# Kernel tuning notes

Hardware: AMD Instinct MI355X
Metric: run time of the kernel (lower is better)

## Reference

```python
import jax, jax.numpy as jnp
import numpy as np
from jax import lax

T, H, K, V, O = 8192, 2048, 512, 512, 2048


def setup_inputs() -> dict:
    key = jax.random.key(0)
    ks = jax.random.split(key, 11)
    s_h = 1.0 / np.sqrt(H)
    s_v = 1.0 / np.sqrt(V)
    return {
        "hidden_state": jax.random.normal(ks[0], (T, H), jnp.float32),
        "Wq": jax.random.normal(ks[1], (H, K), jnp.float32) * s_h,
        "bq": jax.random.normal(ks[2], (K,), jnp.float32) * 0.02,
        "Wk": jax.random.normal(ks[3], (H, K), jnp.float32) * s_h,
        "bk": jax.random.normal(ks[4], (K,), jnp.float32) * 0.02,
        "Wv": jax.random.normal(ks[5], (H, V), jnp.float32) * s_h,
        "bv": jax.random.normal(ks[6], (V,), jnp.float32) * 0.02,
        "Wg": jax.random.normal(ks[7], (H, K), jnp.float32) * s_h,
        "bg": jax.random.normal(ks[8], (K,), jnp.float32) * 0.02,
        "Wo": jax.random.normal(ks[9], (V, O), jnp.float32) * s_v,
        "bo": jax.random.normal(ks[10], (O,), jnp.float32) * 0.02,
    }


def reference(hidden_state, Wq, bq, Wk, bk, Wv, bv, Wg, bg, Wo, bo):
    # Batched projections (torch Linear: x @ W^T + b; here W stored as [in,out])
    q = hidden_state @ Wq + bq                    # [T, K]
    k = jax.nn.sigmoid(hidden_state @ Wk + bk)    # [T, K]
    g = jax.nn.sigmoid(hidden_state @ Wg + bg)    # [T, K]
    v = hidden_state @ Wv + bv                    # [T, V]

    def step(state, qkvg):
        qi, ki, vi, gi = qkvg
        # state: [K, V]; gated decay per key-dim row, then outer-product write
        state = state * gi[:, None] + ki[:, None] * vi[None, :]
        out_i = qi @ state  # == state.T @ qi -> [V]
        return state, out_i

    init = jnp.zeros((K, V), hidden_state.dtype)
    final_state, outs = lax.scan(step, init, (q, k, v, g))  # outs: [T, V]
    output = outs @ Wo + bo                                  # [T, O]
    return output, final_state
```

## Files before the change

### kernel.cpp

```cpp
#include <hip/hip_runtime.h>

#define T_LEN 8192
#define H_DIM 2048
#define K_DIM 512
#define V_DIM 512
#define O_DIM 2048
#define CHUNK 64
#define NCHUNK 128
#define CGROUP 64

typedef short bf16x8 __attribute__((ext_vector_type(8)));
typedef float f32x4 __attribute__((ext_vector_type(4)));

typedef const __attribute__((address_space(1))) void* gptr1_t;
typedef __attribute__((address_space(3))) void* lptr3_t;

__device__ __forceinline__ float b2f(unsigned short u) {
    unsigned int i = ((unsigned int)u) << 16;
    float f;
    __builtin_memcpy(&f, &i, 4);
    return f;
}
__device__ __forceinline__ unsigned short f2b(float f) {
    unsigned int i;
    __builtin_memcpy(&i, &f, 4);
    unsigned int r = (i + 0x7FFFu + ((i >> 16) & 1u)) >> 16;
    return (unsigned short)r;
}
__device__ __forceinline__ float fw(float v) {
    return fminf(fmaxf(v, -1e30f), 1e30f);
}

__global__ __launch_bounds__(256) void conv2bf_k(const float* __restrict__ in,
                                                 unsigned short* __restrict__ out,
                                                 long N) {
    long i = ((long)blockIdx.x * 256 + threadIdx.x) * 8;
    if (i >= N) return;
    unsigned int w[4];
#pragma unroll
    for (int u = 0; u < 4; u++) {
        unsigned short lo = f2b(in[i + 2 * u]);
        unsigned short hi = f2b(in[i + 2 * u + 1]);
        w[u] = (unsigned int)lo | ((unsigned int)hi << 16);
    }
    uint4 pk; pk.x = w[0]; pk.y = w[1]; pk.z = w[2]; pk.w = w[3];
    *(uint4*)(out + i) = pk;
}

__global__ __launch_bounds__(64) void probe_k(int* __restrict__ flag) {
    __shared__ unsigned short As[16 * 32];
    __shared__ unsigned short Bs[16 * 32];
    int tid = threadIdx.x;
    for (int idx = tid; idx < 512; idx += 64) {
        int r = idx >> 5, c = idx & 31;
        float av = (c == 0) ? (float)(r + 1) : (c == 1 ? 1.0f : 0.0f);
        float bv = (c == 0) ? 1.0f : (c == 1 ? (float)(1024 * (r + 1)) : 0.0f);
        As[r * 32 + c] = f2b(av);
        Bs[r * 32 + c] = f2b(bv);
    }
    __syncthreads();
    int ln15 = tid & 15, q4 = (tid & 63) >> 4;
    bf16x8 a = *(const bf16x8*)(As + ln15 * 32 + q4 * 8);
    bf16x8 b = *(const bf16x8*)(Bs + ln15 * 32 + q4 * 8);
    f32x4 acc = {0.f, 0.f, 0.f, 0.f};
    acc = __builtin_amdgcn_mfma_f32_16x16x32_bf16(a, b, acc, 0, 0, 0);
    bool h0 = true, h1 = true;
#pragma unroll
    for (int i = 0; i < 4; i++) {
        float e0 = (float)((q4 * 4 + i + 1) + 1024 * (ln15 + 1));
        float e1 = (float)((ln15 + 1) + 1024 * (q4 * 4 + i + 1));
        h0 = h0 && (acc[i] == e0);
        h1 = h1 && (acc[i] == e1);
    }
    unsigned long long b0 = __ballot(h0 ? 1 : 0);
    unsigned long long b1 = __ballot(h1 ? 1 : 0);
    if (tid == 0) *flag = (b0 == ~0ull) ? 0 : ((b1 == ~0ull) ? 1 : 0);
}

template <int DF>
__global__ __launch_bounds__(256) void transpose_k(const void* __restrict__ in,
                                                   unsigned short* __restrict__ out,
                                                   int R, int C) {
    __shared__ unsigned short tile[32][33];
    int br = blockIdx.x, bc = blockIdx.y;
    int tc = threadIdx.x & 31, tr = threadIdx.x >> 5;
#pragma unroll
    for (int i = 0; i < 4; i++) {
        int r = tr + 8 * i;
        long idx = (long)(br * 32 + r) * C + bc * 32 + tc;
        tile[r][tc] = DF ? f2b(((const float*)in)[idx]) : ((const unsigned short*)in)[idx];
    }
    __syncthreads();
#pragma unroll
    for (int i = 0; i < 4; i++) {
        int r = tr + 8 * i;
        out[(long)(bc * 32 + r) * R + br * 32 + tc] = tile[tc][r];
    }
}

__global__ __launch_bounds__(512, 2) void proj_gemm256_k(const unsigned short* __restrict__ A,
                                                         const unsigned short* __restrict__ WT,
                                                         const float* __restrict__ bq,
                                                         const float* __restrict__ bk,
                                                         const float* __restrict__ bg,
                                                         const float* __restrict__ bv,
                                                         unsigned short* __restrict__ qb,
                                                         unsigned short* __restrict__ kb,
                                                         float* __restrict__ gb,
                                                         unsigned short* __restrict__ vT,
                                                         const int* __restrict__ flagp) {
    __shared__ unsigned short As[2][256 * 64];
    __shared__ unsigned short Bs[2][256 * 64];
    int fl = *flagp;
    int tid = threadIdx.x;
    int lane = tid & 63;
    int ln15 = lane & 15, q4 = lane >> 4;
    int w = tid >> 6;
    int wm = w >> 2, wn = w & 3;
    long m0 = (long)blockIdx.x * 256, n0 = (long)blockIdx.y * 256;

    int idx0 = tid, idx1 = 512 + tid;
    int r0_ = idx0 >> 3, r1_ = idx1 >> 3;
    int c80 = (idx0 & 7) ^ (r0_ & 7);
    int c81 = (idx1 & 7) ^ (r1_ & 7);
    int trA0 = ((r0_ >> 6) & 1) * 128 + (r0_ & 63);
    int trA1 = ((r1_ >> 6) & 1) * 128 + (r1_ & 63);
    int tcB0 = ((r0_ >> 5) & 3) * 64 + (r0_ & 31);
    int tcB1 = ((r1_ >> 5) & 3) * 64 + (r1_ & 31);
    const unsigned short* gA0 = A + (m0 + trA0) * (long)H_DIM + c80 * 8;
    const unsigned short* gA1 = A + (m0 + trA1) * (long)H_DIM + c81 * 8;
    const unsigned short* gB0 = WT + (n0 + tcB0) * (long)H_DIM + c80 * 8;
    const unsigned short* gB1 = WT + (n0 + tcB1) * (long)H_DIM + c81 * 8;
    int ld0 = idx0 * 8, ld1 = idx1 * 8;

#define STAGE_A(buf, half, ks)                                                              \
    do {                                                                                    \
        __builtin_amdgcn_global_load_lds(                                                   \
            (gptr1_t)(const void*)(gA0 + (long)(half) * 64 * H_DIM + (ks)),                 \
            (lptr3_t)(void*)(&As[buf][(half) * 8192 + ld0]), 16, 0, 0);                     \
        __builtin_amdgcn_global_load_lds(                                                   \
            (gptr1_t)(const void*)(gA1 + (long)(half) * 64 * H_DIM + (ks)),                 \
            (lptr3_t)(void*)(&As[buf][(half) * 8192 + ld1]), 16, 0, 0);                     \
    } while (0)
#define STAGE_B(buf, half, ks)                                                              \
    do {                                                                                    \
        __builtin_amdgcn_global_load_lds(                                                   \
            (gptr1_t)(const void*)(gB0 + (long)(half) * 32 * H_DIM + (ks)),                 \
            (lptr3_t)(void*)(&Bs[buf][(half) * 8192 + ld0]), 16, 0, 0);                     \
        __builtin_amdgcn_global_load_lds(                                                   \
            (gptr1_t)(const void*)(gB1 + (long)(half) * 32 * H_DIM + (ks)),                 \
            (lptr3_t)(void*)(&Bs[buf][(half) * 8192 + ld1]), 16, 0, 0);                     \
    } while (0)

    auto LDA = [&](int buf, int im, int s) -> bf16x8 {
        int row = (im >> 2) * 128 + wm * 64 + (im & 3) * 16 + ln15;
        int cb = (s * 64 + q4 * 16) ^ ((row & 7) << 4);
        return *(const bf16x8*)((const unsigned short*)As[buf] + row * 64 + (cb >> 1));
    };
    auto LDB = [&](int buf, int jn, int s) -> bf16x8 {
        int row = (jn >> 1) * 128 + wn * 32 + (jn & 1) * 16 + ln15;
        int cb = (s * 64 + q4 * 16) ^ ((row & 7) << 4);
        return *(const bf16x8*)((const unsigned short*)Bs[buf] + row * 64 + (cb >> 1));
    };

    f32x4 acc[8][4] = {};

    STAGE_A(0, 0, 0);
    STAGE_B(0, 0, 0);
    STAGE_B(0, 1, 0);
    STAGE_A(0, 1, 0);
    STAGE_A(1, 0, 64);
    STAGE_B(1, 0, 64);
    asm volatile("s_waitcnt vmcnt(4)" ::: "memory");
    __builtin_amdgcn_s_barrier();

    int cur = 0;
    for (int kt = 0; kt < H_DIM; kt += 64, cur ^= 1) {
        int k1 = (kt + 64) & (H_DIM - 1);
        int k2 = (kt + 128) & (H_DIM - 1);
        bf16x8 af[4][2], blo[2][2], bhi[2][2];

#pragma unroll
        for (int i = 0; i < 4; i++) { af[i][0] = LDA(cur, i, 0); af[i][1] = LDA(cur, i, 1); }
#pragma unroll
        for (int j = 0; j < 2; j++) { blo[j][0] = LDB(cur, j, 0); blo[j][1] = LDB(cur, j, 1); }
        STAGE_B(cur ^ 1, 1, k1);
        __builtin_amdgcn_s_barrier();
        asm volatile("s_waitcnt lgkmcnt(0)" ::: "memory");
        __builtin_amdgcn_sched_barrier(0);
        __builtin_amdgcn_s_setprio(1);
#pragma unroll
        for (int i = 0; i < 4; i++)
#pragma unroll
            for (int j = 0; j < 2; j++) {
                acc[i][j] = __builtin_amdgcn_mfma_f32_16x16x32_bf16(af[i][0], blo[j][0], acc[i][j], 0, 0, 0);
                acc[i][j] = __builtin_amdgcn_mfma_f32_16x16x32_bf16(af[i][1], blo[j][1], acc[i][j], 0, 0, 0);
            }
        __builtin_amdgcn_s_setprio(0);
        __builtin_amdgcn_s_barrier();

#pragma unroll
        for (int j = 0; j < 2; j++) { bhi[j][0] = LDB(cur, 2 + j, 0); bhi[j][1] = LDB(cur, 2 + j, 1); }
        STAGE_A(cur ^ 1, 1, k1);
        __builtin_amdgcn_s_barrier();
        asm volatile("s_waitcnt lgkmcnt(0)" ::: "memory");
        __builtin_amdgcn_sched_barrier(0);
        __builtin_amdgcn_s_setprio(1);
#pragma unroll
        for (int i = 0; i < 4; i++)
#pragma unroll
            for (int j = 0; j < 2; j++) {
                acc[i][2 + j] = __builtin_amdgcn_mfma_f32_16x16x32_bf16(af[i][0], bhi[j][0], acc[i][2 + j], 0, 0, 0);
                acc[i][2 + j] = __builtin_amdgcn_mfma_f32_16x16x32_bf16(af[i][1], bhi[j][1], acc[i][2 + j], 0, 0, 0);
            }
        __builtin_amdgcn_s_setprio(0);
        __builtin_amdgcn_s_barrier();

#pragma unroll
        for (int i = 0; i < 4; i++) { af[i][0] = LDA(cur, 4 + i, 0); af[i][1] = LDA(cur, 4 + i, 1); }
        STAGE_A(cur, 0, k2);
        __builtin_amdgcn_s_barrier();
        asm volatile("s_waitcnt lgkmcnt(0)" ::: "memory");
        __builtin_amdgcn_sched_barrier(0);
        __builtin_amdgcn_s_setprio(1);
#pragma unroll
        for (int i = 0; i < 4; i++)
#pragma unroll
            for (int j = 0; j < 2; j++) {
                acc[4 + i][2 + j] = __builtin_amdgcn_mfma_f32_16x16x32_bf16(af[i][0], bhi[j][0], acc[4 + i][2 + j], 0, 0, 0);
                acc[4 + i][2 + j] = __builtin_amdgcn_mfma_f32_16x16x32_bf16(af[i][1], bhi[j][1], acc[4 + i][2 + j], 0, 0, 0);
            }
        __builtin_amdgcn_s_setprio(0);
        __builtin_amdgcn_s_barrier();

        STAGE_B(cur, 0, k2);
        __builtin_amdgcn_s_setprio(1);
#pragma unroll
        for (int i = 0; i < 4; i++)
#pragma unroll
            for (int j = 0; j < 2; j++) {
                acc[4 + i][j] = __builtin_amdgcn_mfma_f32_16x16x32_bf16(af[i][0], blo[j][0], acc[4 + i][j], 0, 0, 0);
                acc[4 + i][j] = __builtin_amdgcn_mfma_f32_16x16x32_bf16(af[i][1], blo[j][1], acc[4 + i][j], 0, 0, 0);
            }
        __builtin_amdgcn_s_setprio(0);
        asm volatile("s_waitcnt vmcnt(4)" ::: "memory");
        __builtin_amdgcn_s_barrier();
    }

    int seg = (int)(n0 >> 9);
    int nl0 = (int)(n0 & 511);
    const float* bias = seg == 0 ? bq : seg == 1 ? bk : seg == 2 ? bg : bv;

    if (seg == 3 && fl == 0) {
#pragma unroll
        for (int im = 0; im < 8; im++)
#pragma unroll
            for (int jn = 0; jn < 4; jn++) {
                int nl = nl0 + wn * 64 + (jn >> 1) * 32 + (jn & 1) * 16 + ln15;
                float bsv = bias[nl];
                long mb = m0 + wm * 128 + (im >> 2) * 64 + (im & 3) * 16 + q4 * 4;
                unsigned short h0 = f2b(fw(acc[im][jn][0] + bsv));
                unsigned short h1 = f2b(fw(acc[im][jn][1] + bsv));
                unsigned short h2 = f2b(fw(acc[im][jn][2] + bsv));
                unsigned short h3 = f2b(fw(acc[im][jn][3] + bsv));
                uint2 pk;
                pk.x = (unsigned int)h0 | ((unsigned int)h1 << 16);
                pk.y = (unsigned int)h2 | ((unsigned int)h3 << 16);
                *(uint2*)(vT + (long)nl * T_LEN + mb) = pk;
            }
    } else {
#pragma unroll
        for (int im = 0; im < 8; im++)
#pragma unroll
            for (int jn = 0; jn < 4; jn++)
#pragma unroll
                for (int ii = 0; ii < 4; ii++) {
                    int dm = fl ? ln15 : q4 * 4 + ii;
                    int dn = fl ? q4 * 4 + ii : ln15;
                    long m = m0 + wm * 128 + (im >> 2) * 64 + (im & 3) * 16 + dm;
                    int nl = nl0 + wn * 64 + (jn >> 1) * 32 + (jn & 1) * 16 + dn;
                    float v = fw(acc[im][jn][ii] + bias[nl]);
                    if (seg == 1 || seg == 2) v = 1.0f / (1.0f + __expf(-v));
                    if (seg == 0)
                        qb[m * K_DIM + nl] = f2b(v);
                    else if (seg == 1)
                        kb[m * K_DIM + nl] = f2b(v);
                    else if (seg == 2)
                        gb[m * K_DIM + nl] = v;
                    else
                        vT[(long)nl * T_LEN + m] = f2b(v);
                }
    }
#undef STAGE_A
#undef STAGE_B
}

__global__ __launch_bounds__(256) void gemm_f32_k(const unsigned short* __restrict__ A,
                                                  const unsigned short* __restrict__ BT,
                                                  const float* __restrict__ bias,
                                                  float* __restrict__ out,
                                                  int M, int N, int K,
                                                  const int* __restrict__ flagp) {
    __shared__ unsigned short As[128 * 32];
    __shared__ unsigned short Bs[128 * 32];
    int fl = *flagp;
    int tid = threadIdx.x;
    int lane = tid & 63;
    int w = tid >> 6;
    int ln15 = lane & 15, q4 = lane >> 4;
    int wm = w >> 1, wn = w & 1;
    long m0 = (long)blockIdx.x * 128, n0 = (long)blockIdx.y * 128;

    f32x4 acc[4][4] = {};

    for (int kt = 0; kt < K; kt += 32) {
        __syncthreads();
#pragma unroll
        for (int it = 0; it < 2; it++) {
            int chunk = it * 256 + tid;
            int row = chunk >> 2;
            int col = (chunk & 3) * 8;
            const unsigned short* ga = A + (m0 + row) * (long)K + kt + col;
            const unsigned short* gbp = BT + (n0 + row) * (long)K + kt + col;
            __builtin_amdgcn_global_load_lds((gptr1_t)(const void*)ga,
                                             (lptr3_t)(void*)(As + chunk * 8), 16, 0, 0);
            __builtin_amdgcn_global_load_lds((gptr1_t)(const void*)gbp,
                                             (lptr3_t)(void*)(Bs + chunk * 8), 16, 0, 0);
        }
        __syncthreads();
        bf16x8 a[4], b[4];
#pragma unroll
        for (int i = 0; i < 4; i++)
            a[i] = *(const bf16x8*)(As + (wm * 64 + 16 * i + ln15) * 32 + q4 * 8);
#pragma unroll
        for (int j = 0; j < 4; j++)
            b[j] = *(const bf16x8*)(Bs + (wn * 64 + 16 * j + ln15) * 32 + q4 * 8);
#pragma unroll
        for (int i = 0; i < 4; i++)
#pragma unroll
            for (int j = 0; j < 4; j++)
                acc[i][j] = __builtin_amdgcn_mfma_f32_16x16x32_bf16(a[i], b[j], acc[i][j], 0, 0, 0);
    }

#pragma unroll
    for (int i = 0; i < 4; i++)
#pragma unroll
        for (int j = 0; j < 4; j++)
#pragma unroll
            for (int ii = 0; ii < 4; ii++) {
                int dm = fl ? ln15 : q4 * 4 + ii;
                int dn = fl ? q4 * 4 + ii : ln15;
                long m = m0 + wm * 64 + 16 * i + dm;
                long n = n0 + wn * 64 + 16 * j + dn;
                out[m * N + n] = fw(acc[i][j][ii] + bias[n]);
            }
}

__global__ __launch_bounds__(256) void cumprod_k(const float* __restrict__ g,
                                                 unsigned short* __restrict__ q,
                                                 unsigned short* __restrict__ k,
                                                 unsigned short* __restrict__ khatT,
                                                 float* __restrict__ pend) {
    int c = blockIdx.x;
    int d = blockIdx.y * 256 + threadIdx.x;
    long base = (long)c * CHUNK * K_DIM + d;
    float P = 1.0f;
    for (int s = 0; s < CHUNK; s++) P = fmaxf(P * g[base + (long)s * K_DIM], 1e-37f);
    pend[c * K_DIM + d] = P;
    float Pend = P;
    P = 1.0f;
    for (int s8 = 0; s8 < CHUNK; s8 += 8) {
        unsigned int packed[4];
#pragma unroll
        for (int u = 0; u < 8; u++) {
            int s = s8 + u;
            long idx = base + (long)s * K_DIM;
            P = fmaxf(P * g[idx], 1e-37f);
            float qv = fw(b2f(q[idx]) * P);
            q[idx] = f2b(qv);
            float kv = b2f(k[idx]);
            float kt = kv / P;
            kt = fmaxf(fminf(kt, 3e37f), -3e37f);
            k[idx] = f2b(kt);
            float ratio = Pend / P;
            unsigned short kh = f2b(fw(kv * ratio));
            if (u & 1)
                packed[u >> 1] |= ((unsigned int)kh) << 16;
            else
                packed[u >> 1] = kh;
        }
        uint4 pk;
        pk.x = packed[0]; pk.y = packed[1]; pk.z = packed[2]; pk.w = packed[3];
        *(uint4*)(khatT + (long)d * T_LEN + c * CHUNK + s8) = pk;
    }
}

__global__ __launch_bounds__(256) void scan_k(const unsigned short* __restrict__ khatT,
                                              const unsigned short* __restrict__ vT,
                                              const float* __restrict__ pend,
                                              unsigned short* __restrict__ ST,
                                              float* __restrict__ Sio,
                                              int c0, int cn,
                                              const int* __restrict__ flagp) {
    int fl = *flagp;
    int lane = threadIdx.x & 63, w = threadIdx.x >> 6;
    int ln15 = lane & 15, q4 = lane >> 4;
    int k0 = (blockIdx.x & 15) * 32 + (w & 1) * 16;
    int v0 = (blockIdx.x >> 4) * 32 + (w >> 1) * 16;
    f32x4 acc;
#pragma unroll
    for (int i = 0; i < 4; i++) {
        int dk = fl ? ln15 : q4 * 4 + i;
        int dv = fl ? q4 * 4 + i : ln15;
        acc[i] = Sio[(long)(k0 + dk) * V_DIM + v0 + dv];
    }
    for (int c = c0; c < cn; c++) {
        long cloc = c - c0;
        if (!fl) {
            uint2 pk;
            pk.x = (unsigned int)f2b(fw(acc[0])) | ((unsigned int)f2b(fw(acc[1])) << 16);
            pk.y = (unsigned int)f2b(fw(acc[2])) | ((unsigned int)f2b(fw(acc[3])) << 16);
            *(uint2*)(ST + (cloc * V_DIM + v0 + ln15) * K_DIM + k0 + q4 * 4) = pk;
            float4 pd = *(const float4*)(pend + c * K_DIM + k0 + q4 * 4);
            acc[0] *= pd.x; acc[1] *= pd.y; acc[2] *= pd.z; acc[3] *= pd.w;
        } else {
#pragma unroll
            for (int i = 0; i < 4; i++)
                ST[(cloc * V_DIM + v0 + q4 * 4 + i) * K_DIM + k0 + ln15] = f2b(fw(acc[i]));
            float pd = pend[c * K_DIM + k0 + ln15];
#pragma unroll
            for (int i = 0; i < 4; i++) acc[i] *= pd;
        }
#pragma unroll
        for (int s0 = 0; s0 < CHUNK; s0 += 32) {
            bf16x8 a = *(const bf16x8*)(khatT + (long)(k0 + ln15) * T_LEN + c * CHUNK + s0 + q4 * 8);
            bf16x8 b = *(const bf16x8*)(vT + (long)(v0 + ln15) * T_LEN + c * CHUNK + s0 + q4 * 8);
            acc = __builtin_amdgcn_mfma_f32_16x16x32_bf16(a, b, acc, 0, 0, 0);
        }
    }
#pragma unroll
    for (int i = 0; i < 4; i++) {
        int dk = fl ? ln15 : q4 * 4 + i;
        int dv = fl ? q4 * 4 + i : ln15;
        Sio[(long)(k0 + dk) * V_DIM + v0 + dv] = fw(acc[i]);
    }
}

__global__ __launch_bounds__(256) void copy_state_k(const float* __restrict__ S,
                                                    float* __restrict__ out) {
    long i = (long)blockIdx.x * 1024 + threadIdx.x * 4;
    *(float4*)(out + i) = *(const float4*)(S + i);
}

__global__ __launch_bounds__(256) void intra_k(const unsigned short* __restrict__ qs,
                                               const unsigned short* __restrict__ ks,
                                               const unsigned short* __restrict__ vT,
                                               const unsigned short* __restrict__ ST,
                                               unsigned short* __restrict__ outs,
                                               int c_base,
                                               const int* __restrict__ flagp) {
    __shared__ unsigned short Ab[64 * 72];
    int fl = *flagp;
    long cloc = blockIdx.x >> 1;
    int c = c_base + (int)cloc, h = blockIdx.x & 1;
    int lane = threadIdx.x & 63, w = threadIdx.x >> 6;
    int ln15 = lane & 15, q4 = lane >> 4;
    long t0 = (long)c * CHUNK;

    {
        f32x4 accA[4] = {};
        for (int kk = 0; kk < K_DIM; kk += 32) {
            bf16x8 a = *(const bf16x8*)(qs + (t0 + 16 * w + ln15) * K_DIM + kk + q4 * 8);
#pragma unroll
            for (int j = 0; j < 4; j++) {
                bf16x8 b = *(const bf16x8*)(ks + (t0 + 16 * j + ln15) * K_DIM + kk + q4 * 8);
                accA[j] = __builtin_amdgcn_mfma_f32_16x16x32_bf16(a, b, accA[j], 0, 0, 0);
            }
        }
#pragma unroll
        for (int j = 0; j < 4; j++)
#pragma unroll
            for (int i = 0; i < 4; i++) {
                int dt = fl ? ln15 : q4 * 4 + i;
                int ds = fl ? q4 * 4 + i : ln15;
                int tl = 16 * w + dt;
                int s = 16 * j + ds;
                float av = (s <= tl) ? accA[j][i] : 0.0f;
                Ab[tl * 72 + s] = f2b(fw(av));
            }
    }
    __syncthreads();

    int v0 = h * 256 + w * 64;
    f32x4 acc[4][4] = {};
    for (int kk = 0; kk < K_DIM; kk += 32) {
        bf16x8 a[4], b[4];
#pragma unroll
        for (int i = 0; i < 4; i++)
            a[i] = *(const bf16x8*)(qs + (t0 + 16 * i + ln15) * K_DIM + kk + q4 * 8);
#pragma unroll
        for (int j = 0; j < 4; j++)
            b[j] = *(const bf16x8*)(ST + (cloc * V_DIM + v0 + 16 * j + ln15) * K_DIM + kk + q4 * 8);
#pragma unroll
        for (int i = 0; i < 4; i++)
#pragma unroll
            for (int j = 0; j < 4; j++)
                acc[i][j] = __builtin_amdgcn_mfma_f32_16x16x32_bf16(a[i], b[j], acc[i][j], 0, 0, 0);
    }
#pragma unroll
    for (int s0 = 0; s0 < CHUNK; s0 += 32) {
        bf16x8 a[4], b[4];
#pragma unroll
        for (int i = 0; i < 4; i++)
            a[i] = *(const bf16x8*)(Ab + (16 * i + ln15) * 72 + s0 + q4 * 8);
#pragma unroll
        for (int j = 0; j < 4; j++)
            b[j] = *(const bf16x8*)(vT + (long)(v0 + 16 * j + ln15) * T_LEN + t0 + s0 + q4 * 8);
#pragma unroll
        for (int i = 0; i < 4; i++)
#pragma unroll
            for (int j = 0; j < 4; j++)
                acc[i][j] = __builtin_amdgcn_mfma_f32_16x16x32_bf16(a[i], b[j], acc[i][j], 0, 0, 0);
    }
#pragma unroll
    for (int i = 0; i < 4; i++)
#pragma unroll
        for (int j = 0; j < 4; j++)
#pragma unroll
            for (int ii = 0; ii < 4; ii++) {
                int dt = fl ? ln15 : q4 * 4 + ii;
                int dv = fl ? q4 * 4 + ii : ln15;
                outs[(t0 + 16 * i + dt) * V_DIM + v0 + 16 * j + dv] = f2b(fw(acc[i][j][ii]));
            }
}

extern "C" void kernel_launch(void* const* d_in, const int* in_sizes, int n_in,
                              void* d_out, int out_size, void* d_ws, size_t ws_size,
                              hipStream_t stream) {
    const float* hs = (const float*)d_in[0];
    const float* Wq = (const float*)d_in[1];
    const float* bq = (const float*)d_in[2];
    const float* Wk = (const float*)d_in[3];
    const float* bk = (const float*)d_in[4];
    const float* Wv = (const float*)d_in[5];
    const float* bv = (const float*)d_in[6];
    const float* Wg = (const float*)d_in[7];
    const float* bg = (const float*)d_in[8];
    const float* Wo = (const float*)d_in[9];
    const float* bo = (const float*)d_in[10];

    float* out = (float*)d_out;

    char* ws = (char*)d_ws;
    const size_t MB = 1024 * 1024;
    unsigned short* WT = (unsigned short*)(ws + 0 * MB);
    unsigned short* WoT = (unsigned short*)(ws + 8 * MB);
    unsigned short* qb = (unsigned short*)(ws + 10 * MB);
    unsigned short* kb = (unsigned short*)(ws + 18 * MB);
    unsigned short* vTb = (unsigned short*)(ws + 26 * MB);
    float* gb = (float*)(ws + 34 * MB);
    unsigned short* outsb = (unsigned short*)(ws + 34 * MB);
    unsigned short* khatT = (unsigned short*)(ws + 50 * MB);
    float* pend = (float*)(ws + 58 * MB);
    int* flags = (int*)(ws + 58 * MB + 256 * 1024);
    float* Scarry = (float*)(ws + 59 * MB);
    unsigned short* STb = (unsigned short*)(ws + 60 * MB);
    unsigned short* hsb = (unsigned short*)(ws + 60 * MB);
    float* fsspare = (float*)(ws + 92 * MB);
    (void)ws_size; (void)in_sizes; (void)n_in;

    float* finalst =
        ((long)out_size >= (long)T_LEN * O_DIM + (long)K_DIM * V_DIM)
            ? out + (long)T_LEN * O_DIM
            : fsspare;

    dim3 b256(256);
    hipMemsetAsync(flags, 0, 16, stream);
    probe_k<<<dim3(1), dim3(64), 0, stream>>>(flags);
    conv2bf_k<<<dim3(8192), b256, 0, stream>>>(hs, hsb, (long)T_LEN * H_DIM);
    transpose_k<1><<<dim3(H_DIM / 32, K_DIM / 32), b256, 0, stream>>>(Wq, WT + 0 * 512 * H_DIM, H_DIM, K_DIM);
    transpose_k<1><<<dim3(H_DIM / 32, K_DIM / 32), b256, 0, stream>>>(Wk, WT + 1 * 512 * H_DIM, H_DIM, K_DIM);
    transpose_k<1><<<dim3(H_DIM / 32, K_DIM / 32), b256, 0, stream>>>(Wg, WT + 2 * 512 * H_DIM, H_DIM, K_DIM);
    transpose_k<1><<<dim3(H_DIM / 32, V_DIM / 32), b256, 0, stream>>>(Wv, WT + 3 * 512 * H_DIM, H_DIM, V_DIM);
    transpose_k<1><<<dim3(V_DIM / 32, O_DIM / 32), b256, 0, stream>>>(Wo, WoT, V_DIM, O_DIM);
    proj_gemm256_k<<<dim3(T_LEN / 256, 8), dim3(512), 0, stream>>>(
        hsb, WT, bq, bk, bg, bv, qb, kb, gb, vTb, flags);
    cumprod_k<<<dim3(NCHUNK, K_DIM / 256), b256, 0, stream>>>(gb, qb, kb, khatT, pend);
    hipMemsetAsync(Scarry, 0, (size_t)K_DIM * V_DIM * 4, stream);
    scan_k<<<dim3(256), b256, 0, stream>>>(khatT, vTb, pend, STb, Scarry, 0, CGROUP, flags);
    intra_k<<<dim3(2 * CGROUP), b256, 0, stream>>>(qb, kb, vTb, STb, outsb, 0, flags);
    scan_k<<<dim3(256), b256, 0, stream>>>(khatT, vTb, pend, STb, Scarry, CGROUP, NCHUNK, flags);
    intra_k<<<dim3(2 * CGROUP), b256, 0, stream>>>(qb, kb, vTb, STb, outsb, CGROUP, flags);
    copy_state_k<<<dim3((K_DIM * V_DIM) / 1024), b256, 0, stream>>>(Scarry, finalst);
    gemm_f32_k<<<dim3(T_LEN / 128, O_DIM / 128), b256, 0, stream>>>(
        outsb, WoT, bo, out, T_LEN, O_DIM, V_DIM, flags);
}
```

Baseline: 455.7 us.

## Fuse prep kernels, single-pass scan with prefetch, and 256-tile output GEMM

Merges the bf16 conversion and the five weight transposes into one prep kernel, which saves launches. The chunk scan now runs in a single pass with register prefetch of the next four chunks, removing the two-group split, the carry memset and the state copy kernel. The output projection moves to a 256x256 double-buffered LDS GEMM like the projection kernel, and cumprod caches the gate products in registers. The explicit lgkmcnt waits and sched barriers are replaced with a plain s_barrier macro, which could risk LDS read ordering.

```diff
diff --git a/kernel.cpp b/kernel.cpp
--- a/kernel.cpp
+++ b/kernel.cpp
@@ -7,7 +7,6 @@
 #define O_DIM 2048
 #define CHUNK 64
 #define NCHUNK 128
-#define CGROUP 64
 
 typedef short bf16x8 __attribute__((ext_vector_type(8)));
 typedef float f32x4 __attribute__((ext_vector_type(4)));
@@ -31,21 +30,7 @@
     return fminf(fmaxf(v, -1e30f), 1e30f);
 }
 
-__global__ __launch_bounds__(256) void conv2bf_k(const float* __restrict__ in,
-                                                 unsigned short* __restrict__ out,
-                                                 long N) {
-    long i = ((long)blockIdx.x * 256 + threadIdx.x) * 8;
-    if (i >= N) return;
-    unsigned int w[4];
-#pragma unroll
-    for (int u = 0; u < 4; u++) {
-        unsigned short lo = f2b(in[i + 2 * u]);
-        unsigned short hi = f2b(in[i + 2 * u + 1]);
-        w[u] = (unsigned int)lo | ((unsigned int)hi << 16);
-    }
-    uint4 pk; pk.x = w[0]; pk.y = w[1]; pk.z = w[2]; pk.w = w[3];
-    *(uint4*)(out + i) = pk;
-}
+#define BARX() asm volatile("s_barrier" ::: "memory")
 
 __global__ __launch_bounds__(64) void probe_k(int* __restrict__ flag) {
     __shared__ unsigned short As[16 * 32];
@@ -77,24 +62,53 @@
     if (tid == 0) *flag = (b0 == ~0ull) ? 0 : ((b1 == ~0ull) ? 1 : 0);
 }
 
-template <int DF>
-__global__ __launch_bounds__(256) void transpose_k(const void* __restrict__ in,
-                                                   unsigned short* __restrict__ out,
-                                                   int R, int C) {
+__global__ __launch_bounds__(256) void prep_k(const float* __restrict__ hs,
+                                              unsigned short* __restrict__ hsb,
+                                              const float* __restrict__ Wq,
+                                              const float* __restrict__ Wk,
+                                              const float* __restrict__ Wg,
+                                              const float* __restrict__ Wv,
+                                              const float* __restrict__ Wo,
+                                              unsigned short* __restrict__ WT,
+                                              unsigned short* __restrict__ WoT) {
     __shared__ unsigned short tile[32][33];
-    int br = blockIdx.x, bc = blockIdx.y;
-    int tc = threadIdx.x & 31, tr = threadIdx.x >> 5;
+    long bid = blockIdx.x;
+    int tid = threadIdx.x;
+    if (bid < 8192) {
+        long i = (bid * 256 + tid) * 8;
+        unsigned int wd[4];
+#pragma unroll
+        for (int u = 0; u < 4; u++) {
+            unsigned short lo = f2b(hs[i + 2 * u]);
+            unsigned short hi = f2b(hs[i + 2 * u + 1]);
+            wd[u] = (unsigned int)lo | ((unsigned int)hi << 16);
+        }
+        uint4 pk; pk.x = wd[0]; pk.y = wd[1]; pk.z = wd[2]; pk.w = wd[3];
+        *(uint4*)(hsb + i) = pk;
+        return;
+    }
+    int t = (int)(bid - 8192);
+    int mat = t >> 10, tl = t & 1023;
+    const float* in; unsigned short* outp; int R, C, br, bc;
+    if (mat < 4) {
+        in = mat == 0 ? Wq : mat == 1 ? Wk : mat == 2 ? Wg : Wv;
+        outp = WT + (long)mat * 512 * H_DIM;
+        R = H_DIM; C = 512; br = tl >> 4; bc = tl & 15;
+    } else {
+        in = Wo; outp = WoT; R = V_DIM; C = O_DIM; br = tl & 15; bc = tl >> 4;
+    }
+    int tc = tid & 31, tr = tid >> 5;
 #pragma unroll
     for (int i = 0; i < 4; i++) {
         int r = tr + 8 * i;
         long idx = (long)(br * 32 + r) * C + bc * 32 + tc;
-        tile[r][tc] = DF ? f2b(((const float*)in)[idx]) : ((const unsigned short*)in)[idx];
+        tile[r][tc] = f2b(in[idx]);
     }
     __syncthreads();
 #pragma unroll
     for (int i = 0; i < 4; i++) {
         int r = tr + 8 * i;
-        out[(long)(bc * 32 + r) * R + br * 32 + tc] = tile[tc][r];
+        outp[(long)(bc * 32 + r) * R + br * 32 + tc] = tile[tc][r];
     }
 }
 
@@ -172,7 +186,7 @@
     STAGE_A(1, 0, 64);
     STAGE_B(1, 0, 64);
     asm volatile("s_waitcnt vmcnt(4)" ::: "memory");
-    __builtin_amdgcn_s_barrier();
+    BARX();
 
     int cur = 0;
     for (int kt = 0; kt < H_DIM; kt += 64, cur ^= 1) {
@@ -185,9 +199,7 @@
 #pragma unroll
         for (int j = 0; j < 2; j++) { blo[j][0] = LDB(cur, j, 0); blo[j][1] = LDB(cur, j, 1); }
         STAGE_B(cur ^ 1, 1, k1);
-        __builtin_amdgcn_s_barrier();
-        asm volatile("s_waitcnt lgkmcnt(0)" ::: "memory");
-        __builtin_amdgcn_sched_barrier(0);
+        BARX();
         __builtin_amdgcn_s_setprio(1);
 #pragma unroll
         for (int i = 0; i < 4; i++)
@@ -197,14 +209,12 @@
                 acc[i][j] = __builtin_amdgcn_mfma_f32_16x16x32_bf16(af[i][1], blo[j][1], acc[i][j], 0, 0, 0);
             }
         __builtin_amdgcn_s_setprio(0);
-        __builtin_amdgcn_s_barrier();
+        BARX();
 
 #pragma unroll
         for (int j = 0; j < 2; j++) { bhi[j][0] = LDB(cur, 2 + j, 0); bhi[j][1] = LDB(cur, 2 + j, 1); }
         STAGE_A(cur ^ 1, 1, k1);
-        __builtin_amdgcn_s_barrier();
-        asm volatile("s_waitcnt lgkmcnt(0)" ::: "memory");
-        __builtin_amdgcn_sched_barrier(0);
+        BARX();
         __builtin_amdgcn_s_setprio(1);
 #pragma unroll
         for (int i = 0; i < 4; i++)
@@ -214,14 +224,12 @@
                 acc[i][2 + j] = __builtin_amdgcn_mfma_f32_16x16x32_bf16(af[i][1], bhi[j][1], acc[i][2 + j], 0, 0, 0);
             }
         __builtin_amdgcn_s_setprio(0);
-        __builtin_amdgcn_s_barrier();
+        BARX();
 
 #pragma unroll
         for (int i = 0; i < 4; i++) { af[i][0] = LDA(cur, 4 + i, 0); af[i][1] = LDA(cur, 4 + i, 1); }
         STAGE_A(cur, 0, k2);
-        __builtin_amdgcn_s_barrier();
-        asm volatile("s_waitcnt lgkmcnt(0)" ::: "memory");
-        __builtin_amdgcn_sched_barrier(0);
+        BARX();
         __builtin_amdgcn_s_setprio(1);
 #pragma unroll
         for (int i = 0; i < 4; i++)
@@ -231,7 +239,7 @@
                 acc[4 + i][2 + j] = __builtin_amdgcn_mfma_f32_16x16x32_bf16(af[i][1], bhi[j][1], acc[4 + i][2 + j], 0, 0, 0);
             }
         __builtin_amdgcn_s_setprio(0);
-        __builtin_amdgcn_s_barrier();
+        BARX();
 
         STAGE_B(cur, 0, k2);
         __builtin_amdgcn_s_setprio(1);
@@ -244,7 +252,7 @@
             }
         __builtin_amdgcn_s_setprio(0);
         asm volatile("s_waitcnt vmcnt(4)" ::: "memory");
-        __builtin_amdgcn_s_barrier();
+        BARX();
     }
 
     int seg = (int)(n0 >> 9);
@@ -295,65 +303,158 @@
 #undef STAGE_B
 }
 
-__global__ __launch_bounds__(256) void gemm_f32_k(const unsigned short* __restrict__ A,
-                                                  const unsigned short* __restrict__ BT,
-                                                  const float* __restrict__ bias,
-                                                  float* __restrict__ out,
-                                                  int M, int N, int K,
-                                                  const int* __restrict__ flagp) {
-    __shared__ unsigned short As[128 * 32];
-    __shared__ unsigned short Bs[128 * 32];
+__global__ __launch_bounds__(512, 2) void gemm256_k(const unsigned short* __restrict__ A,
+                                                    const unsigned short* __restrict__ BT,
+                                                    const float* __restrict__ bias,
+                                                    float* __restrict__ out,
+                                                    int N, int KT,
+                                                    const int* __restrict__ flagp) {
+    __shared__ unsigned short As[2][256 * 64];
+    __shared__ unsigned short Bs[2][256 * 64];
     int fl = *flagp;
     int tid = threadIdx.x;
     int lane = tid & 63;
+    int ln15 = lane & 15, q4 = lane >> 4;
     int w = tid >> 6;
-    int ln15 = lane & 15, q4 = lane >> 4;
-    int wm = w >> 1, wn = w & 1;
-    long m0 = (long)blockIdx.x * 128, n0 = (long)blockIdx.y * 128;
-
-    f32x4 acc[4][4] = {};
-
-    for (int kt = 0; kt < K; kt += 32) {
-        __syncthreads();
-#pragma unroll
-        for (int it = 0; it < 2; it++) {
-            int chunk = it * 256 + tid;
-            int row = chunk >> 2;
-            int col = (chunk & 3) * 8;
-            const unsigned short* ga = A + (m0 + row) * (long)K + kt + col;
-            const unsigned short* gbp = BT + (n0 + row) * (long)K + kt + col;
-            __builtin_amdgcn_global_load_lds((gptr1_t)(const void*)ga,
-                                             (lptr3_t)(void*)(As + chunk * 8), 16, 0, 0);
-            __builtin_amdgcn_global_load_lds((gptr1_t)(const void*)gbp,
-                                             (lptr3_t)(void*)(Bs + chunk * 8), 16, 0, 0);
-        }
-        __syncthreads();
-        bf16x8 a[4], b[4];
-#pragma unroll
-        for (int i = 0; i < 4; i++)
-            a[i] = *(const bf16x8*)(As + (wm * 64 + 16 * i + ln15) * 32 + q4 * 8);
-#pragma unroll
-        for (int j = 0; j < 4; j++)
-            b[j] = *(const bf16x8*)(Bs + (wn * 64 + 16 * j + ln15) * 32 + q4 * 8);
-#pragma unroll
-        for (int i = 0; i < 4; i++)
-#pragma unroll
-            for (int j = 0; j < 4; j++)
-                acc[i][j] = __builtin_amdgcn_mfma_f32_16x16x32_bf16(a[i], b[j], acc[i][j], 0, 0, 0);
-    }
-
-#pragma unroll
-    for (int i = 0; i < 4; i++)
-#pragma unroll
-        for (int j = 0; j < 4; j++)
+    int wm = w >> 2, wn = w & 3;
+    long m0 = (long)blockIdx.x * 256, n0 = (long)blockIdx.y * 256;
+
+    int idx0 = tid, idx1 = 512 + tid;
+    int r0_ = idx0 >> 3, r1_ = idx1 >> 3;
+    int c80 = (idx0 & 7) ^ (r0_ & 7);
+    int c81 = (idx1 & 7) ^ (r1_ & 7);
+    int trA0 = ((r0_ >> 6) & 1) * 128 + (r0_ & 63);
+    int trA1 = ((r1_ >> 6) & 1) * 128 + (r1_ & 63);
+    int tcB0 = ((r0_ >> 5) & 3) * 64 + (r0_ & 31);
+    int tcB1 = ((r1_ >> 5) & 3) * 64 + (r1_ & 31);
+    const unsigned short* gA0 = A + (m0 + trA0) * (long)KT + c80 * 8;
+    const unsigned short* gA1 = A + (m0 + trA1) * (long)KT + c81 * 8;
+    const unsigned short* gB0 = BT + (n0 + tcB0) * (long)KT + c80 * 8;
+    const unsigned short* gB1 = BT + (n0 + tcB1) * (long)KT + c81 * 8;
+    int ld0 = idx0 * 8, ld1 = idx1 * 8;
+
+#define STAGE_A(buf, half, ks)                                                              \
+    do {                                                                                    \
+        __builtin_amdgcn_global_load_lds(                                                   \
+            (gptr1_t)(const void*)(gA0 + (long)(half) * 64 * KT + (ks)),                    \
+            (lptr3_t)(void*)(&As[buf][(half) * 8192 + ld0]), 16, 0, 0);                     \
+        __builtin_amdgcn_global_load_lds(                                                   \
+            (gptr1_t)(const void*)(gA1 + (long)(half) * 64 * KT + (ks)),                    \
+            (lptr3_t)(void*)(&As[buf][(half) * 8192 + ld1]), 16, 0, 0);                     \
+    } while (0)
+#define STAGE_B(buf, half, ks)                                                              \
+    do {                                                                                    \
+        __builtin_amdgcn_global_load_lds(                                                   \
+            (gptr1_t)(const void*)(gB0 + (long)(half) * 32 * KT + (ks)),                    \
+            (lptr3_t)(void*)(&Bs[buf][(half) * 8192 + ld0]), 16, 0, 0);                     \
+        __builtin_amdgcn_global_load_lds(                                                   \
+            (gptr1_t)(const void*)(gB1 + (long)(half) * 32 * KT + (ks)),                    \
+            (lptr3_t)(void*)(&Bs[buf][(half) * 8192 + ld1]), 16, 0, 0);                     \
+    } while (0)
+
+    auto LDA = [&](int buf, int im, int s) -> bf16x8 {
+        int row = (im >> 2) * 128 + wm * 64 + (im & 3) * 16 + ln15;
+        int cb = (s * 64 + q4 * 16) ^ ((row & 7) << 4);
+        return *(const bf16x8*)((const unsigned short*)As[buf] + row * 64 + (cb >> 1));
+    };
+    auto LDB = [&](int buf, int jn, int s) -> bf16x8 {
+        int row = (jn >> 1) * 128 + wn * 32 + (jn & 1) * 16 + ln15;
+        int cb = (s * 64 + q4 * 16) ^ ((row & 7) << 4);
+        return *(const bf16x8*)((const unsigned short*)Bs[buf] + row * 64 + (cb >> 1));
+    };
+
+    f32x4 acc[8][4] = {};
+
+    STAGE_A(0, 0, 0);
+    STAGE_B(0, 0, 0);
+    STAGE_B(0, 1, 0);
+    STAGE_A(0, 1, 0);
+    STAGE_A(1, 0, 64);
+    STAGE_B(1, 0, 64);
+    asm volatile("s_waitcnt vmcnt(4)" ::: "memory");
+    BARX();
+
+    int cur = 0;
+    for (int kt = 0; kt < KT; kt += 64, cur ^= 1) {
+        int k1 = (kt + 64) & (KT - 1);
+        int k2 = (kt + 128) & (KT - 1);
+        bf16x8 af[4][2], blo[2][2], bhi[2][2];
+
+#pragma unroll
+        for (int i = 0; i < 4; i++) { af[i][0] = LDA(cur, i, 0); af[i][1] = LDA(cur, i, 1); }
+#pragma unroll
+        for (int j = 0; j < 2; j++) { blo[j][0] = LDB(cur, j, 0); blo[j][1] = LDB(cur, j, 1); }
+        STAGE_B(cur ^ 1, 1, k1);
+        BARX();
+        __builtin_amdgcn_s_setprio(1);
+#pragma unroll
+        for (int i = 0; i < 4; i++)
+#pragma unroll
+            for (int j = 0; j < 2; j++) {
+                acc[i][j] = __builtin_amdgcn_mfma_f32_16x16x32_bf16(af[i][0], blo[j][0], acc[i][j], 0, 0, 0);
+                acc[i][j] = __builtin_amdgcn_mfma_f32_16x16x32_bf16(af[i][1], blo[j][1], acc[i][j], 0, 0, 0);
+            }
+        __builtin_amdgcn_s_setprio(0);
+        BARX();
+
+#pragma unroll
+        for (int j = 0; j < 2; j++) { bhi[j][0] = LDB(cur, 2 + j, 0); bhi[j][1] = LDB(cur, 2 + j, 1); }
+        STAGE_A(cur ^ 1, 1, k1);
+        BARX();
+        __builtin_amdgcn_s_setprio(1);
+#pragma unroll
+        for (int i = 0; i < 4; i++)
+#pragma unroll
+            for (int j = 0; j < 2; j++) {
+                acc[i][2 + j] = __builtin_amdgcn_mfma_f32_16x16x32_bf16(af[i][0], bhi[j][0], acc[i][2 + j], 0, 0, 0);
+                acc[i][2 + j] = __builtin_amdgcn_mfma_f32_16x16x32_bf16(af[i][1], bhi[j][1], acc[i][2 + j], 0, 0, 0);
+            }
+        __builtin_amdgcn_s_setprio(0);
+        BARX();
+
+#pragma unroll
+        for (int i = 0; i < 4; i++) { af[i][0] = LDA(cur, 4 + i, 0); af[i][1] = LDA(cur, 4 + i, 1); }
+        STAGE_A(cur, 0, k2);
+        BARX();
+        __builtin_amdgcn_s_setprio(1);
+#pragma unroll
+        for (int i = 0; i < 4; i++)
+#pragma unroll
+            for (int j = 0; j < 2; j++) {
+                acc[4 + i][2 + j] = __builtin_amdgcn_mfma_f32_16x16x32_bf16(af[i][0], bhi[j][0], acc[4 + i][2 + j], 0, 0, 0);
+                acc[4 + i][2 + j] = __builtin_amdgcn_mfma_f32_16x16x32_bf16(af[i][1], bhi[j][1], acc[4 + i][2 + j], 0, 0, 0);
+            }
+        __builtin_amdgcn_s_setprio(0);
+        BARX();
+
+        STAGE_B(cur, 0, k2);
+        __builtin_amdgcn_s_setprio(1);
+#pragma unroll
+        for (int i = 0; i < 4; i++)
+#pragma unroll
+            for (int j = 0; j < 2; j++) {
+                acc[4 + i][j] = __builtin_amdgcn_mfma_f32_16x16x32_bf16(af[i][0], blo[j][0], acc[4 + i][j], 0, 0, 0);
+                acc[4 + i][j] = __builtin_amdgcn_mfma_f32_16x16x32_bf16(af[i][1], blo[j][1], acc[4 + i][j], 0, 0, 0);
+            }
+        __builtin_amdgcn_s_setprio(0);
+        asm volatile("s_waitcnt vmcnt(4)" ::: "memory");
+        BARX();
+    }
+
+#pragma unroll
+    for (int im = 0; im < 8; im++)
+#pragma unroll
+        for (int jn = 0; jn < 4; jn++)
 #pragma unroll
             for (int ii = 0; ii < 4; ii++) {
                 int dm = fl ? ln15 : q4 * 4 + ii;
                 int dn = fl ? q4 * 4 + ii : ln15;
-                long m = m0 + wm * 64 + 16 * i + dm;
-                long n = n0 + wn * 64 + 16 * j + dn;
-                out[m * N + n] = fw(acc[i][j][ii] + bias[n]);
-            }
+                long m = m0 + wm * 128 + (im >> 2) * 64 + (im & 3) * 16 + dm;
+                long n = n0 + wn * 64 + (jn >> 1) * 32 + (jn & 1) * 16 + dn;
+                out[m * N + n] = fw(acc[im][jn][ii] + bias[n]);
+            }
+#undef STAGE_A
+#undef STAGE_B
 }
 
 __global__ __launch_bounds__(256) void cumprod_k(const float* __restrict__ g,
@@ -364,25 +465,29 @@
     int c = blockIdx.x;
     int d = blockIdx.y * 256 + threadIdx.x;
     long base = (long)c * CHUNK * K_DIM + d;
+    float gv[CHUNK];
+#pragma unroll
+    for (int s = 0; s < CHUNK; s++) gv[s] = g[base + (long)s * K_DIM];
     float P = 1.0f;
-    for (int s = 0; s < CHUNK; s++) P = fmaxf(P * g[base + (long)s * K_DIM], 1e-37f);
+#pragma unroll
+    for (int s = 0; s < CHUNK; s++) { P = fmaxf(P * gv[s], 1e-37f); gv[s] = P; }
     pend[c * K_DIM + d] = P;
     float Pend = P;
-    P = 1.0f;
+#pragma unroll
     for (int s8 = 0; s8 < CHUNK; s8 += 8) {
         unsigned int packed[4];
 #pragma unroll
         for (int u = 0; u < 8; u++) {
             int s = s8 + u;
             long idx = base + (long)s * K_DIM;
-            P = fmaxf(P * g[idx], 1e-37f);
-            float qv = fw(b2f(q[idx]) * P);
+            float Pc = gv[s];
+            float qv = fw(b2f(q[idx]) * Pc);
             q[idx] = f2b(qv);
             float kv = b2f(k[idx]);
-            float kt = kv / P;
+            float kt = kv / Pc;
             kt = fmaxf(fminf(kt, 3e37f), -3e37f);
             k[idx] = f2b(kt);
-            float ratio = Pend / P;
+            float ratio = Pend / Pc;
             unsigned short kh = f2b(fw(kv * ratio));
             if (u & 1)
                 packed[u >> 1] |= ((unsigned int)kh) << 16;
@@ -399,57 +504,73 @@
                                               const unsigned short* __restrict__ vT,
                                               const float* __restrict__ pend,
                                               unsigned short* __restrict__ ST,
-                                              float* __restrict__ Sio,
-                                              int c0, int cn,
+                                              float* __restrict__ fstate,
                                               const int* __restrict__ flagp) {
     int fl = *flagp;
     int lane = threadIdx.x & 63, w = threadIdx.x >> 6;
     int ln15 = lane & 15, q4 = lane >> 4;
     int k0 = (blockIdx.x & 15) * 32 + (w & 1) * 16;
     int v0 = (blockIdx.x >> 4) * 32 + (w >> 1) * 16;
-    f32x4 acc;
+    f32x4 acc = {0.f, 0.f, 0.f, 0.f};
+    const unsigned short* kb_ = khatT + (long)(k0 + ln15) * T_LEN + q4 * 8;
+    const unsigned short* vb_ = vT + (long)(v0 + ln15) * T_LEN + q4 * 8;
+
+    bf16x8 kf0[2], vf0[2], kf1[2], vf1[2], kf2[2], vf2[2], kf3[2], vf3[2];
+    float4 pdv[4];
+    float pds[4];
+
+#define LOADSET(s, c)                                                        \
+    do {                                                                     \
+        long off_ = (long)(c) * CHUNK;                                       \
+        kf##s[0] = *(const bf16x8*)(kb_ + off_);                             \
+        kf##s[1] = *(const bf16x8*)(kb_ + off_ + 32);                        \
+        vf##s[0] = *(const bf16x8*)(vb_ + off_);                             \
+        vf##s[1] = *(const bf16x8*)(vb_ + off_ + 32);                        \
+        if (!fl)                                                             \
+            pdv[s] = *(const float4*)(pend + (c) * K_DIM + k0 + q4 * 4);     \
+        else                                                                 \
+            pds[s] = pend[(c) * K_DIM + k0 + ln15];                          \
+    } while (0)
+
+    LOADSET(0, 0); LOADSET(1, 1); LOADSET(2, 2); LOADSET(3, 3);
+
+#define STEP(s, c)                                                                             \
+    do {                                                                                       \
+        if (!fl) {                                                                             \
+            uint2 pk_;                                                                         \
+            pk_.x = (unsigned int)f2b(fw(acc[0])) | ((unsigned int)f2b(fw(acc[1])) << 16);     \
+            pk_.y = (unsigned int)f2b(fw(acc[2])) | ((unsigned int)f2b(fw(acc[3])) << 16);     \
+            *(uint2*)(ST + ((long)(c) * V_DIM + v0 + ln15) * K_DIM + k0 + q4 * 4) = pk_;       \
+            acc[0] *= pdv[s].x; acc[1] *= pdv[s].y; acc[2] *= pdv[s].z; acc[3] *= pdv[s].w;    \
+        } else {                                                                               \
+            ST[((long)(c) * V_DIM + v0 + q4 * 4 + 0) * K_DIM + k0 + ln15] = f2b(fw(acc[0]));   \
+            ST[((long)(c) * V_DIM + v0 + q4 * 4 + 1) * K_DIM + k0 + ln15] = f2b(fw(acc[1]));   \
+            ST[((long)(c) * V_DIM + v0 + q4 * 4 + 2) * K_DIM + k0 + ln15] = f2b(fw(acc[2]));   \
+            ST[((long)(c) * V_DIM + v0 + q4 * 4 + 3) * K_DIM + k0 + ln15] = f2b(fw(acc[3]));   \
+            acc[0] *= pds[s]; acc[1] *= pds[s]; acc[2] *= pds[s]; acc[3] *= pds[s];            \
+        }                                                                                      \
+        acc = __builtin_amdgcn_mfma_f32_16x16x32_bf16(kf##s[0], vf##s[0], acc, 0, 0, 0);       \
+        acc = __builtin_amdgcn_mfma_f32_16x16x32_bf16(kf##s[1], vf##s[1], acc, 0, 0, 0);       \
+        int cp_ = (c) + 4;                                                                     \
+        if (cp_ > NCHUNK - 1) cp_ = NCHUNK - 1;                                                \
+        LOADSET(s, cp_);                                                                       \
+    } while (0)
+
+    for (int c = 0; c < NCHUNK; c += 4) {
+        STEP(0, c);
+        STEP(1, c + 1);
+        STEP(2, c + 2);
+        STEP(3, c + 3);
+    }
+#undef STEP
+#undef LOADSET
+
 #pragma unroll
     for (int i = 0; i < 4; i++) {
         int dk = fl ? ln15 : q4 * 4 + i;
         int dv = fl ? q4 * 4 + i : ln15;
-        acc[i] = Sio[(long)(k0 + dk) * V_DIM + v0 + dv];
-    }
-    for (int c = c0; c < cn; c++) {
-        long cloc = c - c0;
-        if (!fl) {
-            uint2 pk;
-            pk.x = (unsigned int)f2b(fw(acc[0])) | ((unsigned int)f2b(fw(acc[1])) << 16);
-            pk.y = (unsigned int)f2b(fw(acc[2])) | ((unsigned int)f2b(fw(acc[3])) << 16);
-            *(uint2*)(ST + (cloc * V_DIM + v0 + ln15) * K_DIM + k0 + q4 * 4) = pk;
-            float4 pd = *(const float4*)(pend + c * K_DIM + k0 + q4 * 4);
-            acc[0] *= pd.x; acc[1] *= pd.y; acc[2] *= pd.z; acc[3] *= pd.w;
-        } else {
-#pragma unroll
-            for (int i = 0; i < 4; i++)
-                ST[(cloc * V_DIM + v0 + q4 * 4 + i) * K_DIM + k0 + ln15] = f2b(fw(acc[i]));
-            float pd = pend[c * K_DIM + k0 + ln15];
-#pragma unroll
-            for (int i = 0; i < 4; i++) acc[i] *= pd;
-        }
-#pragma unroll
-        for (int s0 = 0; s0 < CHUNK; s0 += 32) {
-            bf16x8 a = *(const bf16x8*)(khatT + (long)(k0 + ln15) * T_LEN + c * CHUNK + s0 + q4 * 8);
-            bf16x8 b = *(const bf16x8*)(vT + (long)(v0 + ln15) * T_LEN + c * CHUNK + s0 + q4 * 8);
-            acc = __builtin_amdgcn_mfma_f32_16x16x32_bf16(a, b, acc, 0, 0, 0);
-        }
-    }
-#pragma unroll
-    for (int i = 0; i < 4; i++) {
-        int dk = fl ? ln15 : q4 * 4 + i;
-        int dv = fl ? q4 * 4 + i : ln15;
-        Sio[(long)(k0 + dk) * V_DIM + v0 + dv] = fw(acc[i]);
-    }
-}
-
-__global__ __launch_bounds__(256) void copy_state_k(const float* __restrict__ S,
-                                                    float* __restrict__ out) {
-    long i = (long)blockIdx.x * 1024 + threadIdx.x * 4;
-    *(float4*)(out + i) = *(const float4*)(S + i);
+        fstate[(long)(k0 + dk) * V_DIM + v0 + dv] = fw(acc[i]);
+    }
 }
 
 __global__ __launch_bounds__(256) void intra_k(const unsigned short* __restrict__ qs,
@@ -457,12 +578,11 @@
                                                const unsigned short* __restrict__ vT,
                                                const unsigned short* __restrict__ ST,
                                                unsigned short* __restrict__ outs,
-                                               int c_base,
                                                const int* __restrict__ flagp) {
     __shared__ unsigned short Ab[64 * 72];
     int fl = *flagp;
     long cloc = blockIdx.x >> 1;
-    int c = c_base + (int)cloc, h = blockIdx.x & 1;
+    int c = (int)cloc, h = blockIdx.x & 1;
     int lane = threadIdx.x & 63, w = threadIdx.x >> 6;
     int ln15 = lane & 15, q4 = lane >> 4;
     long t0 = (long)c * CHUNK;
@@ -554,19 +674,18 @@
     char* ws = (char*)d_ws;
     const size_t MB = 1024 * 1024;
     unsigned short* WT = (unsigned short*)(ws + 0 * MB);
+    unsigned short* outsb = (unsigned short*)(ws + 0 * MB);
     unsigned short* WoT = (unsigned short*)(ws + 8 * MB);
     unsigned short* qb = (unsigned short*)(ws + 10 * MB);
     unsigned short* kb = (unsigned short*)(ws + 18 * MB);
     unsigned short* vTb = (unsigned short*)(ws + 26 * MB);
-    float* gb = (float*)(ws + 34 * MB);
-    unsigned short* outsb = (unsigned short*)(ws + 34 * MB);
-    unsigned short* khatT = (unsigned short*)(ws + 50 * MB);
-    float* pend = (float*)(ws + 58 * MB);
-    int* flags = (int*)(ws + 58 * MB + 256 * 1024);
-    float* Scarry = (float*)(ws + 59 * MB);
-    unsigned short* STb = (unsigned short*)(ws + 60 * MB);
+    unsigned short* khatT = (unsigned short*)(ws + 34 * MB);
+    float* pend = (float*)(ws + 42 * MB);
+    int* flags = (int*)(ws + 42 * MB + 256 * 1024);
+    float* gb = (float*)(ws + 44 * MB);
+    unsigned short* STb = (unsigned short*)(ws + 44 * MB);
     unsigned short* hsb = (unsigned short*)(ws + 60 * MB);
-    float* fsspare = (float*)(ws + 92 * MB);
+    float* fsspare = (float*)(ws + 108 * MB);
     (void)ws_size; (void)in_sizes; (void)n_in;
 
     float* finalst =
@@ -577,21 +696,12 @@
     dim3 b256(256);
     hipMemsetAsync(flags, 0, 16, stream);
     probe_k<<<dim3(1), dim3(64), 0, stream>>>(flags);
-    conv2bf_k<<<dim3(8192), b256, 0, stream>>>(hs, hsb, (long)T_LEN * H_DIM);
-    transpose_k<1><<<dim3(H_DIM / 32, K_DIM / 32), b256, 0, stream>>>(Wq, WT + 0 * 512 * H_DIM, H_DIM, K_DIM);
-    transpose_k<1><<<dim3(H_DIM / 32, K_DIM / 32), b256, 0, stream>>>(Wk, WT + 1 * 512 * H_DIM, H_DIM, K_DIM);
-    transpose_k<1><<<dim3(H_DIM / 32, K_DIM / 32), b256, 0, stream>>>(Wg, WT + 2 * 512 * H_DIM, H_DIM, K_DIM);
-    transpose_k<1><<<dim3(H_DIM / 32, V_DIM / 32), b256, 0, stream>>>(Wv, WT + 3 * 512 * H_DIM, H_DIM, V_DIM);
-    transpose_k<1><<<dim3(V_DIM / 32, O_DIM / 32), b256, 0, stream>>>(Wo, WoT, V_DIM, O_DIM);
+    prep_k<<<dim3(8192 + 5 * 1024), b256, 0, stream>>>(hs, hsb, Wq, Wk, Wg, Wv, Wo, WT, WoT);
     proj_gemm256_k<<<dim3(T_LEN / 256, 8), dim3(512), 0, stream>>>(
         hsb, WT, bq, bk, bg, bv, qb, kb, gb, vTb, flags);
     cumprod_k<<<dim3(NCHUNK, K_DIM / 256), b256, 0, stream>>>(gb, qb, kb, khatT, pend);
-    hipMemsetAsync(Scarry, 0, (size_t)K_DIM * V_DIM * 4, stream);
-    scan_k<<<dim3(256), b256, 0, stream>>>(khatT, vTb, pend, STb, Scarry, 0, CGROUP, flags);
-    intra_k<<<dim3(2 * CGROUP), b256, 0, stream>>>(qb, kb, vTb, STb, outsb, 0, flags);
-    scan_k<<<dim3(256), b256, 0, stream>>>(khatT, vTb, pend, STb, Scarry, CGROUP, NCHUNK, flags);
-    intra_k<<<dim3(2 * CGROUP), b256, 0, stream>>>(qb, kb, vTb, STb, outsb, CGROUP, flags);
-    copy_state_k<<<dim3((K_DIM * V_DIM) / 1024), b256, 0, stream>>>(Scarry, finalst);
-    gemm_f32_k<<<dim3(T_LEN / 128, O_DIM / 128), b256, 0, stream>>>(
-        outsb, WoT, bo, out, T_LEN, O_DIM, V_DIM, flags);
-}
+    scan_k<<<dim3(256), b256, 0, stream>>>(khatT, vTb, pend, STb, finalst, flags);
+    intra_k<<<dim3(2 * NCHUNK), b256, 0, stream>>>(qb, kb, vTb, STb, outsb, flags);
+    gemm256_k<<<dim3(T_LEN / 256, O_DIM / 256), dim3(512), 0, stream>>>(
+        outsb, WoT, bo, out, O_DIM, V_DIM, flags);
+}
```

Result: faster. 389.7 us (-14.5%).
